# Kernel optimization log

Measured on AMD Instinct MI355X. Metric: run time of the kernel, lower is better.

## Reference

```python
import math
import jax, jax.numpy as jnp
import numpy as np

NQ, NK = 16384, 4096
QDIM, KDIM, MID = 512, 256, 256


def setup_inputs() -> dict:
    key = jax.random.key(0)
    k1, k2, k3, k4, k5, k6, k7, k8 = jax.random.split(key, 8)
    return {
        "global_embeddings": jax.random.normal(k1, (NQ, QDIM), dtype=jnp.float32),
        "substruct_embeddings": jax.random.normal(k2, (NK, KDIM), dtype=jnp.float32),
        "substruct_weight": jax.random.uniform(k3, (NK,), dtype=jnp.float32),
        "mask": jax.random.randint(k4, (NQ, NK), 0, 2, dtype=jnp.int32),
        "Wq": jax.random.normal(k5, (MID, QDIM), dtype=jnp.float32) / math.sqrt(QDIM),
        "bq": jax.random.normal(k6, (MID,), dtype=jnp.float32) * 0.01,
        "Wk": jax.random.normal(k7, (MID, KDIM), dtype=jnp.float32) / math.sqrt(KDIM),
        "bk": jax.random.normal(k8, (MID,), dtype=jnp.float32) * 0.01,
    }


def reference(global_embeddings, substruct_embeddings, substruct_weight, mask, Wq, bq, Wk, bk):
    # Q/K projections (torch Linear: x @ W.T + b)
    Q = global_embeddings @ Wq.T + bq            # [NQ, MID]
    K = substruct_embeddings @ Wk.T + bk         # [NK, MID]
    scores = (Q @ K.T) / math.sqrt(MID)          # [NQ, NK]
    scores = jnp.where(mask == 0, -jnp.inf, scores)
    attn = jax.nn.softmax(scores, axis=-1)       # row-wise stable softmax
    # torch.diag(w) @ E  ==  elementwise row scaling
    V = substruct_weight[:, None] * substruct_embeddings  # [NK, KDIM]
    return attn @ V                              # [NQ, KDIM]
```

## Files before the change

kernel.cpp:

```cpp
#include <hip/hip_runtime.h>
#include <hip/hip_bf16.h>

typedef __bf16 bf16_t;
typedef bf16_t bf16x8 __attribute__((ext_vector_type(8)));
typedef float  f32x4  __attribute__((ext_vector_type(4)));
typedef unsigned long long u64;
typedef unsigned int u32;

#define MFMA16(A,B,C) __builtin_amdgcn_mfma_f32_16x16x32_bf16((A),(B),(C),0,0,0)


static __device__ __forceinline__ void gl_lds16(const bf16_t* g, void* l) {
    __builtin_amdgcn_global_load_lds(
        (const __attribute__((address_space(1))) u32*)(const void*)g,
        (__attribute__((address_space(3))) u32*)l, 16, 0, 0);
}

template<int KA, bool SWZ>
__global__ __launch_bounds__(256)
void proj_kernel(const float* __restrict__ A, const float* __restrict__ W,
                 const float* __restrict__ b, bf16_t* __restrict__ C,
                 float scale)
{
    __shared__ bf16_t Alds[64][40];
    __shared__ bf16_t Wlds[256][40];

    const int t  = threadIdx.x;
    const int w  = t >> 6, l = t & 63, lr = l & 15, lg = l >> 4;
    const int m0 = blockIdx.x * 64;

    f32x4 acc[16];
#pragma unroll
    for (int tt = 0; tt < 16; ++tt) acc[tt] = (f32x4){0.f, 0.f, 0.f, 0.f};

    const int ar  = t >> 2;
    const int ac8 = (t & 3) * 8;

    for (int kb = 0; kb < KA / 32; ++kb) {
        {
            const float* ap = A + (size_t)(m0 + ar) * KA + kb * 32 + ac8;
            float4 a0 = *(const float4*)ap;
            float4 a1 = *(const float4*)(ap + 4);
            bf16x8 av;
            av[0]=(bf16_t)a0.x; av[1]=(bf16_t)a0.y; av[2]=(bf16_t)a0.z; av[3]=(bf16_t)a0.w;
            av[4]=(bf16_t)a1.x; av[5]=(bf16_t)a1.y; av[6]=(bf16_t)a1.z; av[7]=(bf16_t)a1.w;
            *(bf16x8*)&Alds[ar][ac8] = av;
        }
#pragma unroll
        for (int c = 0; c < 4; ++c) {
            int e8 = c * 256 + t;
            int wr = e8 >> 2, wc8 = (e8 & 3) * 8;
            const float* wp = W + (size_t)wr * KA + kb * 32 + wc8;
            float4 w0 = *(const float4*)wp;
            float4 w1 = *(const float4*)(wp + 4);
            bf16x8 wv;
            wv[0]=(bf16_t)w0.x; wv[1]=(bf16_t)w0.y; wv[2]=(bf16_t)w0.z; wv[3]=(bf16_t)w0.w;
            wv[4]=(bf16_t)w1.x; wv[5]=(bf16_t)w1.y; wv[6]=(bf16_t)w1.z; wv[7]=(bf16_t)w1.w;
            *(bf16x8*)&Wlds[wr][wc8] = wv;
        }
        __syncthreads();

        bf16x8 af = *(bf16x8*)&Alds[w * 16 + lr][lg * 8];
#pragma unroll
        for (int tt = 0; tt < 16; ++tt) {
            bf16x8 bfrag = *(bf16x8*)&Wlds[tt * 16 + lr][lg * 8];
            acc[tt] = MFMA16(af, bfrag, acc[tt]);
        }
        __syncthreads();
    }

#pragma unroll
    for (int tt = 0; tt < 16; ++tt) {
        int col = tt * 16 + lr;
        float bias = b[col];
#pragma unroll
        for (int r = 0; r < 4; ++r) {
            int row = m0 + w * 16 + lg * 4 + r;
            int colS = col;
            if (SWZ) colS = (((col >> 3) ^ (row & 7)) << 3) | (col & 7);
            C[(size_t)row * 256 + colS] = (bf16_t)((acc[tt][r] + bias) * scale);
        }
    }
}

__global__ __launch_bounds__(256)
void buildvt_kernel(const float* __restrict__ S, const float* __restrict__ wgt,
                    bf16_t* __restrict__ VT)
{
    int i = blockIdx.x * 256 + threadIdx.x;
    int d = i >> 12, k = i & 4095;
    int kt = (k & ~63) | (((((k >> 3) & 7) ^ (d & 7)) << 3)) | (k & 7);
    VT[i] = (bf16_t)(wgt[kt] * S[(size_t)kt * 256 + d]);
}

template<bool SPLIT>
__global__ __launch_bounds__(512, 2)
void attn_kernel(const bf16_t* __restrict__ Qb, const bf16_t* __restrict__ Kb,
                 const bf16_t* __restrict__ VT, const int* __restrict__ mask,
                 float* __restrict__ out, float* __restrict__ pacc,
                 float* __restrict__ pm, float* __restrict__ pl)
{
    __shared__ __align__(16) char Kraw[2][32768];
    __shared__ __align__(16) char Vraw[2][32768];

    const int t  = threadIdx.x;
    const int w  = t >> 6, l = t & 63, lr = l & 15, lg = l >> 4;
    const int qw = blockIdx.x * 128 + w * 16;
    const int half = SPLIT ? (int)blockIdx.y : 0;
    const int NT   = SPLIT ? 32 : 64;
    const int kb0  = half * NT;

    bf16x8 qf[8];
    {
        const bf16_t* qrow = Qb + (size_t)(qw + lr) * 256;
#pragma unroll
        for (int kk = 0; kk < 8; ++kk)
            qf[kk] = *(const bf16x8*)(qrow + kk * 32 + lg * 8);
    }

    bf16x8 vone;
#pragma unroll
    for (int j = 0; j < 8; ++j) vone[j] = (bf16_t)1.0f;

    f32x4 acc[16];
#pragma unroll
    for (int dt = 0; dt < 16; ++dt) acc[dt] = (f32x4){0.f, 0.f, 0.f, 0.f};
    f32x4 lacc = (f32x4){0.f, 0.f, 0.f, 0.f};
    float mrow = -1e30f;

    auto stage = [&](int kb, char* kd, char* vd) {
#pragma unroll
        for (int i = 0; i < 4; ++i) {
            int row = w * 8 + i * 2 + (l >> 5);
            gl_lds16(Kb + (size_t)(kb * 64 + row) * 256 + (l & 31) * 8,
                     kd + (w * 8 + i * 2) * 512);
        }
#pragma unroll
        for (int i = 0; i < 4; ++i) {
            int d = w * 32 + i * 8 + (l >> 3);
            gl_lds16(VT + (size_t)d * 4096 + kb * 64 + (l & 7) * 8,
                     vd + (w * 32 + i * 8) * 128);
        }
    };

    auto iter = [&](int kb, char* kcur, char* vcur, char* knxt, char* vnxt,
                    bool do_stage) {
        int4 mv[4];
#pragma unroll
        for (int tt = 0; tt < 4; ++tt)
            mv[tt] = *(const int4*)(mask + (size_t)(qw + lr) * 4096
                                    + kb * 64 + tt * 16 + lg * 4);

        if (do_stage) stage(kb + 1, knxt, vnxt);
        __syncthreads();

        f32x4 s[4];
#pragma unroll
        for (int tt = 0; tt < 4; ++tt) {
            f32x4 sv = (f32x4){0.f, 0.f, 0.f, 0.f};
#pragma unroll
            for (int kk = 0; kk < 8; ++kk) {
                bf16x8 kf = *(bf16x8*)(kcur + (((tt * 16 + lr) * 512)
                                | ((((kk * 4 + lg) ^ (lr & 7)) << 4))));
                sv = MFMA16(kf, qf[kk], sv);
            }
            s[tt] = sv;
        }

#pragma unroll
        for (int tt = 0; tt < 4; ++tt) {
            s[tt][0] = mv[tt].x ? s[tt][0] : -1e30f;
            s[tt][1] = mv[tt].y ? s[tt][1] : -1e30f;
            s[tt][2] = mv[tt].z ? s[tt][2] : -1e30f;
            s[tt][3] = mv[tt].w ? s[tt][3] : -1e30f;
        }

        float bm;
        {
            f32x4 m4 = s[0];
#pragma unroll
            for (int tt = 1; tt < 4; ++tt) {
                m4[0] = fmaxf(m4[0], s[tt][0]);
                m4[1] = fmaxf(m4[1], s[tt][1]);
                m4[2] = fmaxf(m4[2], s[tt][2]);
                m4[3] = fmaxf(m4[3], s[tt][3]);
            }
            bm = fmaxf(fmaxf(m4[0], m4[1]), fmaxf(m4[2], m4[3]));
            bm = fmaxf(bm, __shfl_xor(bm, 16));
            bm = fmaxf(bm, __shfl_xor(bm, 32));
        }

        bool need = bm > mrow + 8.f;
        if (__any(need)) {
            float mn = fmaxf(mrow, bm);
            float fr = __expf(mrow - mn);
            mrow = mn;
            float frC[4];
#pragma unroll
            for (int r = 0; r < 4; ++r) frC[r] = __shfl(fr, lg * 4 + r);
#pragma unroll
            for (int r = 0; r < 4; ++r) {
                lacc[r] *= frC[r];
#pragma unroll
                for (int dt = 0; dt < 16; ++dt) acc[dt][r] *= frC[r];
            }
        }

#pragma unroll
        for (int tt = 0; tt < 4; ++tt)
#pragma unroll
            for (int r = 0; r < 4; ++r)
                s[tt][r] = __expf(s[tt][r] - mrow);

        bf16x8 pa[2];
#pragma unroll
        for (int g = 0; g < 2; ++g) {
            u32 x0, x1, y0, y1;
            asm("v_cvt_pk_bf16_f32 %0, %1, %2"
                : "=v"(x0) : "v"(s[2 * g][0]), "v"(s[2 * g][1]));
            asm("v_cvt_pk_bf16_f32 %0, %1, %2"
                : "=v"(x1) : "v"(s[2 * g][2]), "v"(s[2 * g][3]));
            asm("v_cvt_pk_bf16_f32 %0, %1, %2"
                : "=v"(y0) : "v"(s[2 * g + 1][0]), "v"(s[2 * g + 1][1]));
            asm("v_cvt_pk_bf16_f32 %0, %1, %2"
                : "=v"(y1) : "v"(s[2 * g + 1][2]), "v"(s[2 * g + 1][3]));
            asm volatile("v_permlane32_swap_b32 %0, %1" : "+v"(x0), "+v"(y0));
            asm volatile("v_permlane32_swap_b32 %0, %1" : "+v"(x1), "+v"(y1));
            u32 sx0 = (u32)__shfl_xor((int)x0, 16);
            u32 sx1 = (u32)__shfl_xor((int)x1, 16);
            u32 sy0 = (u32)__shfl_xor((int)y0, 16);
            u32 sy1 = (u32)__shfl_xor((int)y1, 16);
            bool evn = (lg & 1) == 0;
            union { u32 uw[4]; bf16x8 v; } pu;
            pu.uw[0] = evn ? x0  : sy0;
            pu.uw[1] = evn ? x1  : sy1;
            pu.uw[2] = evn ? sx0 : y0;
            pu.uw[3] = evn ? sx1 : y1;
            pa[g] = pu.v;
        }

        lacc = MFMA16(pa[0], vone, lacc);
        lacc = MFMA16(pa[1], vone, lacc);
#pragma unroll
        for (int dt = 0; dt < 16; ++dt) {
            int vrow = dt * 16 + lr;
            bf16x8 v0 = *(bf16x8*)(vcur + ((vrow * 128)
                            | ((((0 * 4 + lg) ^ (lr & 7)) << 4))));
            bf16x8 v1 = *(bf16x8*)(vcur + ((vrow * 128)
                            | ((((1 * 4 + lg) ^ (lr & 7)) << 4))));
            acc[dt] = MFMA16(pa[0], v0, acc[dt]);
            acc[dt] = MFMA16(pa[1], v1, acc[dt]);
        }
        __syncthreads();
    };

    stage(kb0, &Kraw[0][0], &Vraw[0][0]);

    for (int tb = 0; tb < NT; tb += 2) {
        iter(kb0 + tb,     &Kraw[0][0], &Vraw[0][0], &Kraw[1][0], &Vraw[1][0],
             true);
        iter(kb0 + tb + 1, &Kraw[1][0], &Vraw[1][0], &Kraw[0][0], &Vraw[0][0],
             tb + 2 < NT);
    }

    if (SPLIT) {
        float* pa_ = pacc + (size_t)half * 16384 * 256;
#pragma unroll
        for (int r = 0; r < 4; ++r) {
            int row = qw + lg * 4 + r;
#pragma unroll
            for (int dt = 0; dt < 16; ++dt)
                pa_[(size_t)row * 256 + dt * 16 + lr] = acc[dt][r];
            if (lr == 0) pl[half * 16384 + row] = lacc[r];
        }
        if (lg == 0 && (w == (l >> 4) || true))
            pm[half * 16384 + qw + lr] = mrow;
    } else {
#pragma unroll
        for (int r = 0; r < 4; ++r) {
            float inv = 1.0f / lacc[r];
#pragma unroll
            for (int dt = 0; dt < 16; ++dt)
                out[(size_t)(qw + lg * 4 + r) * 256 + dt * 16 + lr]
                    = acc[dt][r] * inv;
        }
    }
}

__global__ __launch_bounds__(256)
void combine_kernel(const float* __restrict__ pacc, const float* __restrict__ pm,
                    const float* __restrict__ pl, float* __restrict__ out)
{
    int idx = blockIdx.x * 256 + threadIdx.x;
    int row = idx >> 6, c4 = (idx & 63) * 4;
    float m0 = pm[row], m1 = pm[16384 + row];
    float l0 = pl[row], l1 = pl[16384 + row];
    float m  = fmaxf(m0, m1);
    float a  = __expf(m0 - m), b = __expf(m1 - m);
    float inv = 1.0f / (l0 * a + l1 * b);
    float4 x0 = *(const float4*)(pacc + (size_t)row * 256 + c4);
    float4 x1 = *(const float4*)(pacc + (size_t)16384 * 256 + (size_t)row * 256 + c4);
    float4 o;
    o.x = (x0.x * a + x1.x * b) * inv;
    o.y = (x0.y * a + x1.y * b) * inv;
    o.z = (x0.z * a + x1.z * b) * inv;
    o.w = (x0.w * a + x1.w * b) * inv;
    *(float4*)(out + (size_t)row * 256 + c4) = o;
}

extern "C" void kernel_launch(void* const* d_in, const int* in_sizes, int n_in,
                              void* d_out, int out_size, void* d_ws, size_t ws_size,
                              hipStream_t stream)
{
    const float* gE   = (const float*)d_in[0];
    const float* sE   = (const float*)d_in[1];
    const float* wgt  = (const float*)d_in[2];
    const int*   mask = (const int*)  d_in[3];
    const float* Wq   = (const float*)d_in[4];
    const float* bq   = (const float*)d_in[5];
    const float* Wk   = (const float*)d_in[6];
    const float* bk   = (const float*)d_in[7];
    float* out = (float*)d_out;

    char* ws = (char*)d_ws;
    bf16_t* Qb = (bf16_t*)ws;
    bf16_t* Kb = (bf16_t*)(ws + 8388608);
    bf16_t* VT = (bf16_t*)(ws + 10485760);
    float*  pacc = (float*)(ws + 12582912);
    float*  pm   = (float*)(ws + 46137344);
    float*  pl   = (float*)(ws + 46268416);
    const size_t need_full = 46399488;
    const size_t need_min  = 12582912;

    if (ws_size < need_min) return;

    proj_kernel<512, false><<<dim3(256, 1), 256, 0, stream>>>(gE, Wq, bq, Qb, 0.0625f);
    proj_kernel<256, true ><<<dim3(64, 1), 256, 0, stream>>>(sE, Wk, bk, Kb, 1.0f);
    buildvt_kernel<<<4096, 256, 0, stream>>>(sE, wgt, VT);

    if (ws_size >= need_full) {
        attn_kernel<true><<<dim3(128, 2), 512, 0, stream>>>(
            Qb, Kb, VT, mask, out, pacc, pm, pl);
        combine_kernel<<<4096, 256, 0, stream>>>(pacc, pm, pl, out);
    } else {
        attn_kernel<false><<<dim3(128, 1), 512, 0, stream>>>(
            Qb, Kb, VT, mask, out, nullptr, nullptr, nullptr);
    }
}
```

Measured before the change: 215.8 us.

## Software-pipeline attention loop so next tile's QK overlaps current PV

Splits the per-tile body into QK, softmax and PV stages and reorders them across iterations. Each step now computes the next tile's scores and the current tile's PV product back to back, then does the softmax. K and V loads are staged separately one tile ahead, and there is one barrier per tile instead of two. It also raises wave priority around the MFMA block with s_setprio, aiming to hide softmax latency and load waits behind matrix work. The cost is more live registers (scores plus the P fragments carried across iterations) and a more complex prologue and epilogue.

```diff
diff --git a/kernel.cpp b/kernel.cpp
--- a/kernel.cpp
+++ b/kernel.cpp
@@ -127,14 +127,22 @@
     for (int dt = 0; dt < 16; ++dt) acc[dt] = (f32x4){0.f, 0.f, 0.f, 0.f};
     f32x4 lacc = (f32x4){0.f, 0.f, 0.f, 0.f};
     float mrow = -1e30f;
-
-    auto stage = [&](int kb, char* kd, char* vd) {
+    bf16x8 pa[2];
+
+    char* const K0 = &Kraw[0][0];
+    char* const K1 = &Kraw[1][0];
+    char* const V0 = &Vraw[0][0];
+    char* const V1 = &Vraw[1][0];
+
+    auto stageK = [&](int kb, char* kd) {
 #pragma unroll
         for (int i = 0; i < 4; ++i) {
             int row = w * 8 + i * 2 + (l >> 5);
             gl_lds16(Kb + (size_t)(kb * 64 + row) * 256 + (l & 31) * 8,
                      kd + (w * 8 + i * 2) * 512);
         }
+    };
+    auto stageV = [&](int kb, char* vd) {
 #pragma unroll
         for (int i = 0; i < 4; ++i) {
             int d = w * 32 + i * 8 + (l >> 3);
@@ -143,18 +151,7 @@
         }
     };
 
-    auto iter = [&](int kb, char* kcur, char* vcur, char* knxt, char* vnxt,
-                    bool do_stage) {
-        int4 mv[4];
-#pragma unroll
-        for (int tt = 0; tt < 4; ++tt)
-            mv[tt] = *(const int4*)(mask + (size_t)(qw + lr) * 4096
-                                    + kb * 64 + tt * 16 + lg * 4);
-
-        if (do_stage) stage(kb + 1, knxt, vnxt);
-        __syncthreads();
-
-        f32x4 s[4];
+    auto qk = [&](char* kcur, f32x4 (&s)[4]) {
 #pragma unroll
         for (int tt = 0; tt < 4; ++tt) {
             f32x4 sv = (f32x4){0.f, 0.f, 0.f, 0.f};
@@ -166,7 +163,24 @@
             }
             s[tt] = sv;
         }
-
+    };
+
+    auto pv = [&](char* vcur) {
+        lacc = MFMA16(pa[0], vone, lacc);
+        lacc = MFMA16(pa[1], vone, lacc);
+#pragma unroll
+        for (int dt = 0; dt < 16; ++dt) {
+            int vrow = dt * 16 + lr;
+            bf16x8 v0 = *(bf16x8*)(vcur + ((vrow * 128)
+                            | ((((0 * 4 + lg) ^ (lr & 7)) << 4))));
+            bf16x8 v1 = *(bf16x8*)(vcur + ((vrow * 128)
+                            | ((((1 * 4 + lg) ^ (lr & 7)) << 4))));
+            acc[dt] = MFMA16(pa[0], v0, acc[dt]);
+            acc[dt] = MFMA16(pa[1], v1, acc[dt]);
+        }
+    };
+
+    auto softmax = [&](int4 (&mv)[4], f32x4 (&s)[4]) {
 #pragma unroll
         for (int tt = 0; tt < 4; ++tt) {
             s[tt][0] = mv[tt].x ? s[tt][0] : -1e30f;
@@ -174,7 +188,6 @@
             s[tt][2] = mv[tt].z ? s[tt][2] : -1e30f;
             s[tt][3] = mv[tt].w ? s[tt][3] : -1e30f;
         }
-
         float bm;
         {
             f32x4 m4 = s[0];
@@ -189,7 +202,6 @@
             bm = fmaxf(bm, __shfl_xor(bm, 16));
             bm = fmaxf(bm, __shfl_xor(bm, 32));
         }
-
         bool need = bm > mrow + 8.f;
         if (__any(need)) {
             float mn = fmaxf(mrow, bm);
@@ -205,14 +217,12 @@
                 for (int dt = 0; dt < 16; ++dt) acc[dt][r] *= frC[r];
             }
         }
-
 #pragma unroll
         for (int tt = 0; tt < 4; ++tt)
 #pragma unroll
             for (int r = 0; r < 4; ++r)
                 s[tt][r] = __expf(s[tt][r] - mrow);
 
-        bf16x8 pa[2];
 #pragma unroll
         for (int g = 0; g < 2; ++g) {
             u32 x0, x1, y0, y1;
@@ -238,29 +248,54 @@
             pu.uw[3] = evn ? sx1 : y1;
             pa[g] = pu.v;
         }
-
-        lacc = MFMA16(pa[0], vone, lacc);
-        lacc = MFMA16(pa[1], vone, lacc);
-#pragma unroll
-        for (int dt = 0; dt < 16; ++dt) {
-            int vrow = dt * 16 + lr;
-            bf16x8 v0 = *(bf16x8*)(vcur + ((vrow * 128)
-                            | ((((0 * 4 + lg) ^ (lr & 7)) << 4))));
-            bf16x8 v1 = *(bf16x8*)(vcur + ((vrow * 128)
-                            | ((((1 * 4 + lg) ^ (lr & 7)) << 4))));
-            acc[dt] = MFMA16(pa[0], v0, acc[dt]);
-            acc[dt] = MFMA16(pa[1], v1, acc[dt]);
-        }
+    };
+
+    stageK(kb0, K0);
+    stageV(kb0, V0);
+    __syncthreads();
+    {
+        int4 mv[4];
+#pragma unroll
+        for (int tt = 0; tt < 4; ++tt)
+            mv[tt] = *(const int4*)(mask + (size_t)(qw + lr) * 4096
+                                    + kb0 * 64 + tt * 16 + lg * 4);
+        f32x4 s[4];
+        qk(K0, s);
+        softmax(mv, s);
+    }
+    stageK(kb0 + 1, K1);
+    __syncthreads();
+
+    for (int tb = 0; tb < NT - 1; ++tb) {
+        char* kQ = (tb & 1) ? K0 : K1;
+        char* vP = (tb & 1) ? V1 : V0;
+        char* kS = (tb & 1) ? K1 : K0;
+        char* vS = (tb & 1) ? V0 : V1;
+        const int kb = kb0 + tb;
+
+        int4 mv[4];
+#pragma unroll
+        for (int tt = 0; tt < 4; ++tt)
+            mv[tt] = *(const int4*)(mask + (size_t)(qw + lr) * 4096
+                                    + (kb + 1) * 64 + tt * 16 + lg * 4);
+
+        if (tb + 2 < NT) stageK(kb + 2, kS);
+        stageV(kb + 1, vS);
+
+        __builtin_amdgcn_s_setprio(1);
+        f32x4 s[4];
+        qk(kQ, s);
+        pv(vP);
+        __builtin_amdgcn_s_setprio(0);
+
+        softmax(mv, s);
+
         __syncthreads();
-    };
-
-    stage(kb0, &Kraw[0][0], &Vraw[0][0]);
-
-    for (int tb = 0; tb < NT; tb += 2) {
-        iter(kb0 + tb,     &Kraw[0][0], &Vraw[0][0], &Kraw[1][0], &Vraw[1][0],
-             true);
-        iter(kb0 + tb + 1, &Kraw[1][0], &Vraw[1][0], &Kraw[0][0], &Vraw[0][0],
-             tb + 2 < NT);
+    }
+
+    {
+        char* vP = ((NT - 1) & 1) ? V1 : V0;
+        pv(vP);
     }
 
     if (SPLIT) {
@@ -273,8 +308,7 @@
                 pa_[(size_t)row * 256 + dt * 16 + lr] = acc[dt][r];
             if (lr == 0) pl[half * 16384 + row] = lacc[r];
         }
-        if (lg == 0 && (w == (l >> 4) || true))
-            pm[half * 16384 + qw + lr] = mrow;
+        if (l < 16) pm[half * 16384 + qw + lr] = mrow;
     } else {
 #pragma unroll
         for (int r = 0; r < 4; ++r) {
```

Measured after the change: 187.7 us. -13.0%, faster.
